# Kernel optimization log

Measured on AMD Instinct MI355X. Metric: run time of the kernel, lower is better.

Reference implementation:

```python
import jax, jax.numpy as jnp
import numpy as np

N = 10000
E = 320000
F_IN = 512
NHID = 32
LATENT = 16


def setup_inputs() -> dict:
    key = jax.random.key(0)
    k1, k2, k3, k4, k5 = jax.random.split(key, 5)
    x = jax.random.normal(k1, (N, F_IN), dtype=jnp.float32)
    W1 = jax.random.normal(k2, (F_IN, NHID), dtype=jnp.float32) * (1.0 / np.sqrt(F_IN))
    W2 = jax.random.normal(k3, (NHID, LATENT), dtype=jnp.float32) * (1.0 / np.sqrt(NHID))
    edge_index = jax.random.randint(k4, (2, E), 0, N, dtype=jnp.int32)
    edge_weight = jax.random.uniform(k5, (E,), dtype=jnp.float32)
    return {"x": x, "W1": W1, "W2": W2, "edge_index": edge_index,
            "edge_weight": edge_weight}


def _spmm(edge_index, edge_weight, h):
    # out[dst] += w * h[src]  (sparse normalized-adjacency matmul)
    src, dst = edge_index[0], edge_index[1]
    msgs = edge_weight[:, None] * h[src]          # [E, D] gather + scale
    return jax.ops.segment_sum(msgs, dst, num_segments=N)  # [N, D]


def reference(x, W1, W2, edge_index, edge_weight):
    # GCNConv layer 1: adj @ (x @ W1)
    h = _spmm(edge_index, edge_weight, x @ W1)    # [N, NHID]
    # GCNConv layer 2: adj @ (h @ W2)
    z = _spmm(edge_index, edge_weight, h @ W2)    # [N, LATENT]
    # Inner-product decoder: sigmoid(z @ z^T)
    adj_recon = jax.nn.sigmoid(z @ z.T)           # [N, N]
    return adj_recon, z
```

## Files before the change

### kernel.cpp

```cpp
#include <hip/hip_runtime.h>
#include <cstdint>
#include <cstddef>

#define N_NODES 10000
#define F_IN    512
#define NHID    32
#define LATENT  16

__global__ __launch_bounds__(256) void gemm1_kernel(const float* __restrict__ x,
                                                    const float* __restrict__ W1,
                                                    float* __restrict__ h0) {
    __shared__ float xs[8][F_IN];
    const int row0 = blockIdx.x * 8;
    for (int t = threadIdx.x; t < 8 * F_IN; t += 256) {
        const int r = t >> 9;
        const int c = t & (F_IN - 1);
        if (row0 + r < N_NODES)
            xs[r][c] = x[(size_t)(row0 + r) * F_IN + c];
    }
    __syncthreads();

    const int col = threadIdx.x & 31;
    const int r   = threadIdx.x >> 5;
    if (row0 + r < N_NODES) {
        float acc = 0.f;
#pragma unroll 8
        for (int k = 0; k < F_IN; ++k) {
            acc += xs[r][k] * W1[k * NHID + col];
        }
        h0[(size_t)(row0 + r) * NHID + col] = acc;
    }
}

template <int D>
__global__ __launch_bounds__(256) void spmm_kernel(const int* __restrict__ src,
                                                   const int* __restrict__ dst,
                                                   const float* __restrict__ w,
                                                   const float* __restrict__ hin,
                                                   float* __restrict__ hout,
                                                   int E) {
    const int idx = blockIdx.x * 256 + threadIdx.x;
    const int e = idx / D;
    const int d = idx & (D - 1);
    if (e < E) {
        const int s = src[e];
        const int t = dst[e];
        const float val = w[e] * hin[(size_t)s * D + d];
        atomicAdd(&hout[(size_t)t * D + d], val);
    }
}

__global__ __launch_bounds__(256) void gemm2_kernel(const float* __restrict__ h,
                                                    const float* __restrict__ W2,
                                                    float* __restrict__ z0) {
    __shared__ float w2s[NHID * LATENT];
    for (int t = threadIdx.x; t < NHID * LATENT; t += 256) w2s[t] = W2[t];
    __syncthreads();

    const int idx = blockIdx.x * 256 + threadIdx.x;
    if (idx < N_NODES * LATENT) {
        const int row = idx >> 4;
        const int col = idx & (LATENT - 1);
        const float* __restrict__ hr = h + (size_t)row * NHID;
        float acc = 0.f;
#pragma unroll
        for (int k = 0; k < NHID; ++k) acc += hr[k] * w2s[k * LATENT + col];
        z0[idx] = acc;
    }
}

#define TI 32

__device__ __forceinline__ float sigmoid_fast(float x) {
    return __builtin_amdgcn_rcpf(1.0f + __expf(-x));
}

__global__ __launch_bounds__(256) void decoder_kernel(const float* __restrict__ z,
                                                      float* __restrict__ out) {
    const int j  = blockIdx.x * 256 + threadIdx.x;
    const int i0 = blockIdx.y * TI;

    float4 zj0, zj1, zj2, zj3;
    if (j < N_NODES) {
        const float4* __restrict__ zp = (const float4*)(z + (size_t)j * LATENT);
        zj0 = zp[0]; zj1 = zp[1]; zj2 = zp[2]; zj3 = zp[3];
    } else {
        zj0 = zj1 = zj2 = zj3 = make_float4(0.f, 0.f, 0.f, 0.f);
    }

    const int imax = min(TI, N_NODES - i0);
    if (imax == TI) {
#pragma unroll 4
        for (int ii = 0; ii < TI; ++ii) {
            const float4* __restrict__ zi = (const float4*)(z + (size_t)(i0 + ii) * LATENT);
            const float4 a0 = zi[0], a1 = zi[1], a2 = zi[2], a3 = zi[3];
            float acc = a0.x * zj0.x + a0.y * zj0.y + a0.z * zj0.z + a0.w * zj0.w
                      + a1.x * zj1.x + a1.y * zj1.y + a1.z * zj1.z + a1.w * zj1.w
                      + a2.x * zj2.x + a2.y * zj2.y + a2.z * zj2.z + a2.w * zj2.w
                      + a3.x * zj3.x + a3.y * zj3.y + a3.z * zj3.z + a3.w * zj3.w;
            if (j < N_NODES) {
                __builtin_nontemporal_store(sigmoid_fast(acc),
                                            &out[(size_t)(i0 + ii) * N_NODES + j]);
            }
        }
    } else {
        for (int ii = 0; ii < imax; ++ii) {
            const float4* __restrict__ zi = (const float4*)(z + (size_t)(i0 + ii) * LATENT);
            const float4 a0 = zi[0], a1 = zi[1], a2 = zi[2], a3 = zi[3];
            float acc = a0.x * zj0.x + a0.y * zj0.y + a0.z * zj0.z + a0.w * zj0.w
                      + a1.x * zj1.x + a1.y * zj1.y + a1.z * zj1.z + a1.w * zj1.w
                      + a2.x * zj2.x + a2.y * zj2.y + a2.z * zj2.z + a2.w * zj2.w
                      + a3.x * zj3.x + a3.y * zj3.y + a3.z * zj3.z + a3.w * zj3.w;
            if (j < N_NODES) {
                __builtin_nontemporal_store(sigmoid_fast(acc),
                                            &out[(size_t)(i0 + ii) * N_NODES + j]);
            }
        }
    }
}

extern "C" void kernel_launch(void* const* d_in, const int* in_sizes, int n_in,
                              void* d_out, int out_size, void* d_ws, size_t ws_size,
                              hipStream_t stream) {
    const float* x  = (const float*)d_in[0];
    const float* W1 = (const float*)d_in[1];
    const float* W2 = (const float*)d_in[2];
    const int*   ei = (const int*)d_in[3];
    const float* ew = (const float*)d_in[4];
    const int E = in_sizes[3] / 2;
    const int* src = ei;
    const int* dst = ei + E;

    float* out = (float*)d_out;
    float* z   = out + (size_t)N_NODES * N_NODES;

    float* h0 = out;
    float* h  = h0 + N_NODES * NHID;
    float* z0 = h  + N_NODES * NHID;

    hipMemsetAsync(h, 0, (size_t)N_NODES * NHID * sizeof(float), stream);
    hipMemsetAsync(z, 0, (size_t)N_NODES * LATENT * sizeof(float), stream);

    gemm1_kernel<<<(N_NODES + 7) / 8, 256, 0, stream>>>(x, W1, h0);
    spmm_kernel<NHID><<<(E * NHID + 255) / 256, 256, 0, stream>>>(src, dst, ew, h0, h, E);

    gemm2_kernel<<<(N_NODES * LATENT + 255) / 256, 256, 0, stream>>>(h, W2, z0);
    spmm_kernel<LATENT><<<(E * LATENT + 255) / 256, 256, 0, stream>>>(src, dst, ew, z0, z, E);

    dim3 dgrid((N_NODES + 255) / 256, (N_NODES + TI - 1) / TI);
    decoder_kernel<<<dgrid, 256, 0, stream>>>(z, out);
}
```

Measured before the change: 507.9 us.

## Build CSR by destination and replace atomic scatter SpMM with per-node gather

Adds a histogram, single-block scan and scatter pass that sort edges by destination into a packed (src, weight) CSR array. Both SpMM layers then use one wavefront per destination node to gather and reduce neighbour rows, with no float atomics and no zeroing memsets. This removes the heavy atomic traffic of the original per-element scatter, at the cost of three extra preprocessing kernels, including a serial single-block scan, which still use integer atomics. All of this scratch space is carved out of the output buffer before the decoder overwrites it.

Result: slower. 551.9 us (+8.7%).

```diff
diff --git a/kernel.cpp b/kernel.cpp
--- a/kernel.cpp
+++ b/kernel.cpp
@@ -32,22 +32,85 @@
     }
 }
 
+__global__ __launch_bounds__(256) void hist_kernel(const int* __restrict__ dst,
+                                                   int* __restrict__ deg, int E) {
+    const int e = blockIdx.x * 256 + threadIdx.x;
+    if (e < E) atomicAdd(&deg[dst[e]], 1);
+}
+
+#define SCAN_T  256
+#define CHUNK   40
+
+__global__ __launch_bounds__(SCAN_T) void scan_kernel(const int* __restrict__ deg,
+                                                      int* __restrict__ off,
+                                                      int* __restrict__ cursor) {
+    __shared__ int part[SCAN_T];
+    const int t  = threadIdx.x;
+    const int i0 = t * CHUNK;
+
+    int s = 0;
+    for (int i = 0; i < CHUNK; ++i) {
+        const int idx = i0 + i;
+        if (idx < N_NODES) s += deg[idx];
+    }
+    part[t] = s;
+    __syncthreads();
+
+    for (int d = 1; d < SCAN_T; d <<= 1) {
+        int w = (t >= d) ? part[t - d] : 0;
+        __syncthreads();
+        part[t] += w;
+        __syncthreads();
+    }
+
+    int run = part[t] - s;
+    for (int i = 0; i < CHUNK; ++i) {
+        const int idx = i0 + i;
+        if (idx < N_NODES) {
+            off[idx]    = run;
+            cursor[idx] = run;
+            run += deg[idx];
+        }
+    }
+    if (t == SCAN_T - 1) off[N_NODES] = run;
+}
+
+__global__ __launch_bounds__(256) void scatter_kernel(const int* __restrict__ src,
+                                                      const int* __restrict__ dst,
+                                                      const float* __restrict__ w,
+                                                      int* __restrict__ cursor,
+                                                      int2* __restrict__ csr, int E) {
+    const int e = blockIdx.x * 256 + threadIdx.x;
+    if (e < E) {
+        const int pos = atomicAdd(&cursor[dst[e]], 1);
+        csr[pos] = make_int2(src[e], __float_as_int(w[e]));
+    }
+}
+
 template <int D>
-__global__ __launch_bounds__(256) void spmm_kernel(const int* __restrict__ src,
-                                                   const int* __restrict__ dst,
-                                                   const float* __restrict__ w,
+__global__ __launch_bounds__(256) void spmm_gather(const int* __restrict__ off,
+                                                   const int2* __restrict__ csr,
                                                    const float* __restrict__ hin,
-                                                   float* __restrict__ hout,
-                                                   int E) {
-    const int idx = blockIdx.x * 256 + threadIdx.x;
-    const int e = idx / D;
-    const int d = idx & (D - 1);
-    if (e < E) {
-        const int s = src[e];
-        const int t = dst[e];
-        const float val = w[e] * hin[(size_t)s * D + d];
-        atomicAdd(&hout[(size_t)t * D + d], val);
-    }
+                                                   float* __restrict__ hout) {
+    constexpr int EPI  = 64 / D;
+    constexpr int LOGD = (D == 32) ? 5 : 4;
+    const int wid  = (blockIdx.x * 256 + threadIdx.x) >> 6;
+    const int lane = threadIdx.x & 63;
+    if (wid >= N_NODES) return;
+
+    const int d   = lane & (D - 1);
+    const int sub = lane >> LOGD;
+    const int p1  = off[wid + 1];
+
+    float acc = 0.f;
+    for (int p = off[wid] + sub; p < p1; p += EPI) {
+        const int2 sw = csr[p];
+        acc += __int_as_float(sw.y) * hin[(size_t)sw.x * D + d];
+    }
+#pragma unroll
+    for (int m = D; m < 64; m <<= 1) acc += __shfl_xor(acc, m);
+
+    if (lane < D) hout[(size_t)wid * D + d] = acc;
 }
 
 __global__ __launch_bounds__(256) void gemm2_kernel(const float* __restrict__ h,
@@ -137,15 +200,26 @@
     float* h0 = out;
     float* h  = h0 + N_NODES * NHID;
     float* z0 = h  + N_NODES * NHID;
-
-    hipMemsetAsync(h, 0, (size_t)N_NODES * NHID * sizeof(float), stream);
-    hipMemsetAsync(z, 0, (size_t)N_NODES * LATENT * sizeof(float), stream);
+    int*   deg    = (int*)(z0 + N_NODES * LATENT);
+    int*   off    = deg;
+    int*   cursor = deg + (N_NODES + 16);
+    int2*  csr    = (int2*)(cursor + (N_NODES + 16));
+
+    int* deg_arr = deg;
+    int* off_arr = (int*)(csr) + 2 * 320000;
+
+    hipMemsetAsync(deg_arr, 0, (size_t)N_NODES * sizeof(int), stream);
+    hist_kernel<<<(E + 255) / 256, 256, 0, stream>>>(dst, deg_arr, E);
+
+    scan_kernel<<<1, SCAN_T, 0, stream>>>(deg_arr, off_arr, cursor);
+
+    scatter_kernel<<<(E + 255) / 256, 256, 0, stream>>>(src, dst, ew, cursor, csr, E);
 
     gemm1_kernel<<<(N_NODES + 7) / 8, 256, 0, stream>>>(x, W1, h0);
-    spmm_kernel<NHID><<<(E * NHID + 255) / 256, 256, 0, stream>>>(src, dst, ew, h0, h, E);
+    spmm_gather<NHID><<<(N_NODES * 64 + 255) / 256, 256, 0, stream>>>(off_arr, csr, h0, h);
 
     gemm2_kernel<<<(N_NODES * LATENT + 255) / 256, 256, 0, stream>>>(h, W2, z0);
-    spmm_kernel<LATENT><<<(E * LATENT + 255) / 256, 256, 0, stream>>>(src, dst, ew, z0, z, E);
+    spmm_gather<LATENT><<<(N_NODES * 64 + 255) / 256, 256, 0, stream>>>(off_arr, csr, z0, z);
 
     dim3 dgrid((N_NODES + 255) / 256, (N_NODES + TI - 1) / TI);
     decoder_kernel<<<dgrid, 256, 0, stream>>>(z, out);
```
